# Optimization experiments

Hardware: AMD Instinct MI355X
Metric: run time of the kernel (lower is better)

The kernel has to match this reference:

```python
import jax, jax.numpy as jnp
import numpy as np

N = 4096       # num nodes
E = 131072     # num edges (avg degree 32)
IN = 256
HID = 512
OUT = 64


def _linear_params(k, fan_in, fan_out):
    kw, kb = jax.random.split(k)
    s = 1.0 / np.sqrt(fan_in)
    W = jax.random.uniform(kw, (fan_in, fan_out), jnp.float32, -s, s)
    b = jax.random.uniform(kb, (fan_out,), jnp.float32, -s, s)
    return W, b


def setup_inputs() -> dict:
    key = jax.random.key(0)
    ks = jax.random.split(key, 8)
    x = jax.random.normal(ks[0], (N, IN), jnp.float32)
    edge_index = jax.random.randint(ks[1], (2, E), 0, N, jnp.int32)
    ego_W, ego_b = _linear_params(ks[2], IN, HID)
    cut_W, cut_b = _linear_params(ks[3], IN, HID)
    glob_W, glob_b = _linear_params(ks[4], IN, HID)
    fc_W, fc_b = _linear_params(ks[5], 3 * HID, OUT)
    return dict(x=x, edge_index=edge_index, ego_W=ego_W, ego_b=ego_b,
                cut_W=cut_W, cut_b=cut_b, glob_W=glob_W, glob_b=glob_b,
                fc_W=fc_W, fc_b=fc_b)


def reference(x, edge_index, ego_W, ego_b, cut_W, cut_b, glob_W, glob_b, fc_W, fc_b):
    src, dst = edge_index[0], edge_index[1]
    n = x.shape[0]

    # --- extract_ego_subgraph: mean of x over the unique 2-hop in-neighborhood
    # (k_hop_subgraph flow='source_to_target': walk edges backward), incl. self.
    # B[t, s] = 1 iff edge s -> t exists.
    B = jnp.zeros((n, n), jnp.float32).at[dst, src].set(1.0)
    eye = jnp.eye(n, dtype=jnp.float32)
    reach = ((eye + B + B @ B) > 0).astype(jnp.float32)   # [N, N] bool-as-float
    ego_feat = (reach @ x) / reach.sum(axis=1, keepdims=True)  # counts >= 1 (self)

    # --- extract_cut_subgraph: drop a random half of the edges, then mean of
    # target features over kept out-edges per source node; fallback to x.
    perm = jax.random.permutation(jax.random.key(42), E)
    keep = jnp.ones(E, bool).at[perm[: E // 2]].set(False).astype(x.dtype)  # [E]
    sums = jax.ops.segment_sum(x[dst] * keep[:, None], src, num_segments=n)
    cnt = jax.ops.segment_sum(keep, src, num_segments=n)
    cut_feat = jnp.where((cnt > 0)[:, None], sums / jnp.maximum(cnt, 1.0)[:, None], x)

    # --- MessagePassingLayer: relu(scatter_add(linear(x)[src] -> dst))
    def mp(feat, W, b):
        h = feat @ W + b
        agg = jax.ops.segment_sum(h[src], dst, num_segments=n)
        return jax.nn.relu(agg)

    ego_enc = mp(ego_feat, ego_W, ego_b)
    cut_enc = mp(cut_feat, cut_W, cut_b)
    glob_enc = x @ glob_W + glob_b

    combined = jnp.concatenate([ego_enc, cut_enc, glob_enc], axis=-1)  # [N, 3H]
    out = combined @ fc_W + fc_b
    return jax.nn.log_softmax(out, axis=1)
```

## Files before the change

kernel.cpp:

```cpp
#include <hip/hip_runtime.h>

#define NN 4096
#define NE 131072
#define DIN 256
#define DHID 512
#define DOUT 64
#define DCAT 1536
#define NBINS 65536
#define HALF_E 65536

typedef __attribute__((ext_vector_type(8))) short short8;
typedef __attribute__((ext_vector_type(4))) float f32x4;

__device__ inline unsigned short bf16rne(float f){
  unsigned u = __float_as_uint(f);
  unsigned r = u + 0x7FFFu + ((u>>16)&1u);
  return (unsigned short)(r>>16);
}
__device__ inline float bf2f(unsigned short u){ return __uint_as_float(((unsigned)u)<<16); }

struct K2 { unsigned a, b; };
__host__ __device__ constexpr unsigned rotl32(unsigned x, unsigned d){ return (x<<d)|(x>>(32u-d)); }
__host__ __device__ constexpr K2 tf2x32(unsigned k0, unsigned k1, unsigned x0, unsigned x1){
  unsigned k2 = k0 ^ k1 ^ 0x1BD11BDAu;
  x0 += k0; x1 += k1;
  x0+=x1; x1=rotl32(x1,13); x1^=x0;
  x0+=x1; x1=rotl32(x1,15); x1^=x0;
  x0+=x1; x1=rotl32(x1,26); x1^=x0;
  x0+=x1; x1=rotl32(x1, 6); x1^=x0;
  x0+=k1; x1+=k2+1u;
  x0+=x1; x1=rotl32(x1,17); x1^=x0;
  x0+=x1; x1=rotl32(x1,29); x1^=x0;
  x0+=x1; x1=rotl32(x1,16); x1^=x0;
  x0+=x1; x1=rotl32(x1,24); x1^=x0;
  x0+=k2; x1+=k0+2u;
  x0+=x1; x1=rotl32(x1,13); x1^=x0;
  x0+=x1; x1=rotl32(x1,15); x1^=x0;
  x0+=x1; x1=rotl32(x1,26); x1^=x0;
  x0+=x1; x1=rotl32(x1, 6); x1^=x0;
  x0+=k0; x1+=k1+3u;
  x0+=x1; x1=rotl32(x1,17); x1^=x0;
  x0+=x1; x1=rotl32(x1,29); x1^=x0;
  x0+=x1; x1=rotl32(x1,16); x1^=x0;
  x0+=x1; x1=rotl32(x1,24); x1^=x0;
  x0+=k1; x1+=k2+4u;
  x0+=x1; x1=rotl32(x1,13); x1^=x0;
  x0+=x1; x1=rotl32(x1,15); x1^=x0;
  x0+=x1; x1=rotl32(x1,26); x1^=x0;
  x0+=x1; x1=rotl32(x1, 6); x1^=x0;
  x0+=k2; x1+=k0+5u;
  return K2{x0,x1};
}
static_assert(tf2x32(0u,0u,0u,2u).a==4146024105u, "threefry mismatch o0");
static_assert(tf2x32(0u,0u,0u,2u).b==2718843009u, "threefry mismatch o1");
static_assert(tf2x32(0u,0u,1u,3u).a==967050713u,  "threefry mismatch o0b");
static_assert(tf2x32(0u,0u,1u,3u).b==1272950319u, "threefry mismatch o1b");

constexpr K2 E0 = tf2x32(0u,42u,0u,0u);
constexpr K2 E1 = tf2x32(0u,42u,0u,1u);
constexpr unsigned SK1A = E1.a, SK1B = E1.b;
constexpr K2 F1 = tf2x32(E0.a,E0.b,0u,1u);
constexpr unsigned SK2A = F1.a, SK2B = F1.b;

#define MED_CAP 64

__global__ void genkeysdeg_k(const int* __restrict__ ei,
                             unsigned* __restrict__ keys1, unsigned* __restrict__ keys2,
                             unsigned* __restrict__ hist1, unsigned* __restrict__ hist2,
                             unsigned* __restrict__ indeg, unsigned* __restrict__ outdeg,
                             unsigned* __restrict__ bits){
  unsigned e = blockIdx.x*256u + threadIdx.x;
  K2 r1 = tf2x32(SK1A, SK1B, 0u, e);
  unsigned k1 = r1.a ^ r1.b;
  K2 r2 = tf2x32(SK2A, SK2B, 0u, e);
  unsigned k2 = r2.a ^ r2.b;
  keys1[e] = k1; keys2[e] = k2;
  atomicAdd(&hist1[k1>>16], 1u);
  atomicAdd(&hist2[k2>>16], 1u);
  unsigned s = (unsigned)ei[e], d = (unsigned)ei[NE+e];
  atomicAdd(&outdeg[s], 1u);
  atomicAdd(&indeg[d], 1u);
  atomicOr(&bits[d*128 + (s>>5)], 1u << (s&31));
  if (e < NN) atomicOr(&bits[e*128 + (e>>5)], 1u << (e&31));
}

__global__ void scanA_k(const unsigned* __restrict__ in0, const unsigned* __restrict__ in1,
                        const unsigned* __restrict__ in2, const unsigned* __restrict__ in3,
                        unsigned* __restrict__ o0, unsigned* __restrict__ o1,
                        unsigned* __restrict__ o2, unsigned* __restrict__ o3,
                        unsigned* __restrict__ bsum){
  int y = blockIdx.y;
  int n = (y<2) ? NBINS : NN;
  if ((int)blockIdx.x*256 >= n) return;
  const unsigned* in = y==0?in0 : y==1?in1 : y==2?in2 : in3;
  unsigned* o        = y==0?o0  : y==1?o1  : y==2?o2  : o3;
  __shared__ unsigned s[256];
  int t = threadIdx.x; unsigned i = blockIdx.x*256u + t;
  unsigned v = in[i]; s[t] = v; __syncthreads();
  for (int off=1; off<256; off<<=1){
    unsigned u = (t>=off)?s[t-off]:0u; __syncthreads();
    s[t]+=u; __syncthreads();
  }
  o[i] = s[t]-v;
  if (t==255) bsum[y*256 + blockIdx.x] = s[255];
}
__global__ void scanB_k(unsigned* __restrict__ bsum){
  __shared__ unsigned s[256];
  int y = blockIdx.x, t = threadIdx.x;
  int nb = (y<2) ? 256 : 16;
  unsigned* b = bsum + y*256;
  unsigned v = (t<nb)?b[t]:0u; s[t]=v; __syncthreads();
  for (int off=1; off<256; off<<=1){
    unsigned u=(t>=off)?s[t-off]:0u; __syncthreads();
    s[t]+=u; __syncthreads();
  }
  if (t<nb) b[t]=s[t]-v;
}
__global__ void scanC_k(unsigned* __restrict__ o0, unsigned* __restrict__ o1,
                        unsigned* __restrict__ o2, unsigned* __restrict__ o3,
                        unsigned* __restrict__ c0, unsigned* __restrict__ c1,
                        unsigned* __restrict__ c2, unsigned* __restrict__ c3,
                        const unsigned* __restrict__ bsum){
  int y = blockIdx.y;
  int n = (y<2) ? NBINS : NN;
  if ((int)blockIdx.x*256 >= n) return;
  unsigned* o = y==0?o0 : y==1?o1 : y==2?o2 : o3;
  unsigned* c = y==0?c0 : y==1?c1 : y==2?c2 : c3;
  unsigned i = blockIdx.x*256u + threadIdx.x;
  unsigned v = o[i] + bsum[y*256 + blockIdx.x];
  o[i]=v; c[i]=v;
}

__global__ void med1_k(const unsigned* __restrict__ prefix2, const unsigned* __restrict__ hist2,
                       unsigned* __restrict__ med){
  unsigned h = blockIdx.x*256u + threadIdx.x;
  unsigned p = prefix2[h], n = hist2[h];
  if (p <= HALF_E && HALF_E < p + n){ med[0] = h; med[1] = p; }
}

__global__ void scat1_k(const unsigned* __restrict__ keys1, unsigned* __restrict__ cursor,
                        unsigned* __restrict__ slow, unsigned* __restrict__ stb){
  int e = blockIdx.x*256 + threadIdx.x;
  unsigned k = keys1[e];
  unsigned p = atomicAdd(&cursor[k>>16], 1u);
  slow[p] = k & 0xFFFFu; stb[p] = (unsigned)e;
}
__global__ void rank1_k(const unsigned* __restrict__ keys1, const unsigned* __restrict__ prefix,
                        const unsigned* __restrict__ hist, const unsigned* __restrict__ slow,
                        const unsigned* __restrict__ stb, const unsigned* __restrict__ keys2,
                        unsigned* __restrict__ rank1, unsigned* __restrict__ med){
  int e = blockIdx.x*256 + threadIdx.x;
  unsigned k = keys1[e], h = k>>16, lo = k & 0xFFFFu, tb = (unsigned)e;
  unsigned base = prefix[h], n = hist[h], r = 0;
  for (unsigned j=0;j<n;j++){
    unsigned l2 = slow[base+j], t2 = stb[base+j];
    if (l2 < lo || (l2==lo && t2 < tb)) r++;
  }
  unsigned rk = base + r;
  rank1[e] = rk;
  unsigned k2 = keys2[rk];
  if ((k2>>16) == med[0]){
    unsigned idx = atomicAdd(&med[2], 1u);
    if (idx < MED_CAP){ med[8+idx] = k2 & 0xFFFFu; med[72+idx] = rk; }
  }
}
__global__ void med3_k(unsigned* __restrict__ med){
  int t = threadIdx.x;
  unsigned n = med[2]; if (n > MED_CAP) n = MED_CAP;
  unsigned qcut = HALF_E - med[1];
  if (t < (int)n){
    unsigned lo = med[8+t], rk = med[72+t], pos = 0;
    for (unsigned j=0;j<n;j++){
      unsigned lj = med[8+j], rj = med[72+j];
      if (lj < lo || (lj==lo && rj < rk)) pos++;
    }
    if (pos == qcut){ med[3] = lo; med[4] = rk; }
  }
}

__global__ void scatter_edges_k(const int* __restrict__ ei, const unsigned* __restrict__ rank1,
                                const unsigned* __restrict__ keys2, const unsigned* __restrict__ med,
                                unsigned* __restrict__ curin, unsigned* __restrict__ curout,
                                unsigned* __restrict__ in_list, unsigned* __restrict__ out_list){
  int e = blockIdx.x*256 + threadIdx.x;
  unsigned s = (unsigned)ei[e], d = (unsigned)ei[NE+e];
  unsigned rk = rank1[e], k2 = keys2[rk];
  unsigned h = k2>>16, lo = k2 & 0xFFFFu;
  unsigned hs = med[0], loc = med[3], rkc = med[4];
  unsigned keep = (h > hs) || (h == hs && (lo > loc || (lo == loc && rk >= rkc)));
  unsigned p = atomicAdd(&curin[d], 1u);  in_list[p] = s;
  unsigned q = atomicAdd(&curout[s], 1u); out_list[q] = d | (keep<<31);
}

__global__ void reach_k(const unsigned* __restrict__ bits, const unsigned* __restrict__ in_off,
                        const unsigned* __restrict__ in_list, const unsigned* __restrict__ indeg,
                        unsigned* __restrict__ reach, float* __restrict__ cntinv){
  __shared__ int ws2[2];
  int i = blockIdx.x, t = threadIdx.x;
  unsigned off = in_off[i], deg = indeg[i];
  unsigned acc = bits[i*128 + t];
  for (unsigned j=0;j<deg;j++) acc |= bits[in_list[off+j]*128 + t];
  reach[i*128 + t] = acc;
  int c = __popc(acc);
  for (int o=32;o>0;o>>=1) c += __shfl_xor(c, o, 64);
  if ((t&63)==0) ws2[t>>6] = c;
  __syncthreads();
  if (t==0) cntinv[i] = 1.0f / (float)(ws2[0]+ws2[1]);
}

__device__ inline void tconv(const float* __restrict__ src, unsigned short* __restrict__ dst,
                             int R, int C, int r0, int c0){
  __shared__ unsigned short tile[64][72];
  int t = threadIdx.x;
  int tr = t>>2, tc = (t&3)*16;
  #pragma unroll
  for (int u=0;u<16;u++)
    tile[tr][tc+u] = bf16rne(src[(size_t)(r0+tr)*C + c0 + tc + u]);
  __syncthreads();
  unsigned short v[16];
  #pragma unroll
  for (int u=0;u<16;u++) v[u] = tile[tc+u][tr];
  uint4* vv = (uint4*)v;
  uint4* o = (uint4*)&dst[(size_t)(c0+tr)*R + r0 + tc];
  o[0] = vv[0]; o[1] = vv[1];
}
__global__ void convall_k(const float* __restrict__ x, unsigned short* __restrict__ x_bf,
                          unsigned short* __restrict__ xT_bf,
                          const float* __restrict__ W0, unsigned short* __restrict__ WT0,
                          const float* __restrict__ W1, unsigned short* __restrict__ WT1,
                          const float* __restrict__ W2, unsigned short* __restrict__ WT2,
                          const float* __restrict__ fcW, unsigned short* __restrict__ fcWT){
  int b = blockIdx.x, t = threadIdx.x;
  if (b < 1024){
    int i = b*256 + t;
    float4 f = ((const float4*)x)[i];
    uint2 o;
    o.x = (unsigned)bf16rne(f.x) | ((unsigned)bf16rne(f.y)<<16);
    o.y = (unsigned)bf16rne(f.z) | ((unsigned)bf16rne(f.w)<<16);
    ((uint2*)x_bf)[i] = o;
  } else if (b < 1280){
    int idx = b - 1024;
    tconv(x, xT_bf, NN, DIN, (idx>>2)*64, (idx&3)*64);
  } else if (b < 1376){
    int idx = b - 1280;
    int z = idx >> 5, tl = idx & 31;
    const float* src = z==0?W0 : z==1?W1 : W2;
    unsigned short* dst = z==0?WT0 : z==1?WT1 : WT2;
    tconv(src, dst, DIN, DHID, (tl>>3)*64, (tl&7)*64);
  } else {
    int by = b - 1376;
    tconv(fcW, fcWT, DCAT, DOUT, by*64, 0);
  }
}

__global__ void bitgemm_k(const unsigned* __restrict__ reach, const unsigned short* __restrict__ xT,
                          float* __restrict__ pbuf){
  __shared__ __align__(16) unsigned short bt[4][64*32];
  int t = threadIdx.x, w = t>>6, l = t&63;
  int m0 = blockIdx.x*64, n0 = blockIdx.y*64;
  int kbase = blockIdx.z*(NN/4);
  int srow = t>>2, sg = t&3;
  int arow = m0 + 16*w + (l&15);
  int lg = l>>4;
  f32x4 acc[4];
  #pragma unroll
  for (int c=0;c<4;c++) acc[c] = f32x4{0.f,0.f,0.f,0.f};

  for (int it=0; it<8; ++it){
    int kk = kbase + it*128;
    __syncthreads();
    #pragma unroll
    for (int s=0;s<4;s++){
      uint4 v = *(const uint4*)&xT[(size_t)(n0+srow)*NN + kk + 32*s + sg*8];
      *(uint4*)&bt[s][srow*32 + ((sg ^ (srow&3))*8)] = v;
    }
    __syncthreads();
    unsigned rw[4];
    *(uint4*)rw = *(const uint4*)&reach[(size_t)arow*128 + (kk>>5)];
    #pragma unroll
    for (int s=0;s<4;s++){
      unsigned byte = (rw[s] >> (8*lg)) & 0xFFu;
      union { short8 s8; unsigned u[4]; } af;
      #pragma unroll
      for (int pp=0;pp<4;pp++){
        unsigned b0 = (byte>>(2*pp))&1u, b1 = (byte>>(2*pp+1))&1u;
        af.u[pp] = b0*0x3F80u | b1*0x3F800000u;
      }
      #pragma unroll
      for (int c=0;c<4;c++){
        int brow = 16*c + (l&15);
        short8 bf = *(const short8*)&bt[s][brow*32 + ((lg ^ (brow&3))*8)];
        acc[c] = __builtin_amdgcn_mfma_f32_16x16x32_bf16(af.s8, bf, acc[c], 0,0,0);
      }
    }
  }
  size_t zoff = (size_t)blockIdx.z*NN*DIN;
  #pragma unroll
  for (int c=0;c<4;c++){
    #pragma unroll
    for (int r=0;r<4;r++){
      int row = m0 + 16*w + 4*lg + r;
      int col = n0 + 16*c + (l&15);
      pbuf[zoff + (size_t)row*DIN + col] = acc[c][r];
    }
  }
}

__global__ void redcut_k(const float* __restrict__ pbuf, const float* __restrict__ cntinv,
                         unsigned short* __restrict__ ego_bf,
                         const float* __restrict__ x, const unsigned* __restrict__ out_off,
                         const unsigned* __restrict__ outdeg, const unsigned* __restrict__ out_list,
                         unsigned short* __restrict__ cut_bf){
  int b = blockIdx.x, t = threadIdx.x;
  if (b < 1024){
    int g = b*256 + t;
    const size_t S = (size_t)NN*DIN/4;
    const float4* p4 = (const float4*)pbuf;
    float4 a = p4[g], bb = p4[g+S], c = p4[g+2*S], d = p4[g+3*S];
    int row = (g*4)>>8;
    float ci = cntinv[row];
    float vx = (a.x+bb.x+c.x+d.x)*ci, vy = (a.y+bb.y+c.y+d.y)*ci;
    float vz = (a.z+bb.z+c.z+d.z)*ci, vw = (a.w+bb.w+c.w+d.w)*ci;
    uint2 o;
    o.x = (unsigned)bf16rne(vx) | ((unsigned)bf16rne(vy)<<16);
    o.y = (unsigned)bf16rne(vz) | ((unsigned)bf16rne(vw)<<16);
    ((uint2*)ego_bf)[g] = o;
  } else {
    int s = b - 1024;
    unsigned off = out_off[s], deg = outdeg[s];
    float acc = 0.f; int cnt = 0;
    for (unsigned j=0;j<deg;j++){
      unsigned p = out_list[off+j];
      if (p >> 31){ cnt++; acc += x[(p & 0xFFFFu)*DIN + t]; }
    }
    float v = cnt ? acc / (float)cnt : x[s*DIN + t];
    cut_bf[(size_t)s*DIN + t] = bf16rne(v);
  }
}

__global__ void aggfeat_k(const unsigned short* __restrict__ ego_bf, const unsigned short* __restrict__ cut_bf,
                          const unsigned* __restrict__ in_off, const unsigned* __restrict__ indeg,
                          const unsigned* __restrict__ in_list,
                          unsigned short* __restrict__ aggE, unsigned short* __restrict__ aggC){
  int i = blockIdx.x, t = threadIdx.x;
  unsigned off = in_off[i], deg = indeg[i];
  float ae = 0.f, ac = 0.f;
  for (unsigned j=0;j<deg;j++){
    unsigned s = in_list[off+j];
    ae += bf2f(ego_bf[(size_t)s*DIN + t]);
    ac += bf2f(cut_bf[(size_t)s*DIN + t]);
  }
  aggE[(size_t)i*DIN + t] = bf16rne(ae);
  aggC[(size_t)i*DIN + t] = bf16rne(ac);
}

__global__ void gemm3_k(const unsigned short* __restrict__ aggE, const unsigned short* __restrict__ aggC,
                        const unsigned short* __restrict__ xbf,
                        const unsigned short* __restrict__ WTe, const unsigned short* __restrict__ WTc,
                        const unsigned short* __restrict__ WTg,
                        const float* __restrict__ eb, const float* __restrict__ cb, const float* __restrict__ gb,
                        const unsigned* __restrict__ indeg, unsigned short* __restrict__ hcat){
  __shared__ __align__(16) unsigned short at[4][64*32];
  __shared__ __align__(16) unsigned short bt[4][64*32];
  int z = blockIdx.z;
  const unsigned short* A  = z==0? aggE : z==1? aggC : xbf;
  const unsigned short* BT = z==0? WTe  : z==1? WTc  : WTg;
  const float* bias        = z==0? eb   : z==1? cb   : gb;
  int t = threadIdx.x, w = t>>6, l = t&63;
  int n0 = blockIdx.x*64, m0 = blockIdx.y*64;
  int srow = t>>2, sg = t&3;
  int lg = l>>4;
  f32x4 acc[4];
  #pragma unroll
  for (int c=0;c<4;c++) acc[c] = f32x4{0.f,0.f,0.f,0.f};

  for (int it=0; it<2; ++it){
    int kk = it*128;
    __syncthreads();
    #pragma unroll
    for (int s=0;s<4;s++){
      uint4 va = *(const uint4*)&A [(size_t)(m0+srow)*DIN + kk + 32*s + sg*8];
      uint4 vb = *(const uint4*)&BT[(size_t)(n0+srow)*DIN + kk + 32*s + sg*8];
      *(uint4*)&at[s][srow*32 + ((sg ^ (srow&3))*8)] = va;
      *(uint4*)&bt[s][srow*32 + ((sg ^ (srow&3))*8)] = vb;
    }
    __syncthreads();
    int ar = 16*w + (l&15);
    #pragma unroll
    for (int s=0;s<4;s++){
      short8 af = *(const short8*)&at[s][ar*32 + ((lg ^ (ar&3))*8)];
      #pragma unroll
      for (int c=0;c<4;c++){
        int brow = 16*c + (l&15);
        short8 bf = *(const short8*)&bt[s][brow*32 + ((lg ^ (brow&3))*8)];
        acc[c] = __builtin_amdgcn_mfma_f32_16x16x32_bf16(af, bf, acc[c], 0,0,0);
      }
    }
  }
  #pragma unroll
  for (int c=0;c<4;c++){
    #pragma unroll
    for (int r=0;r<4;r++){
      int row = m0 + 16*w + 4*lg + r;
      int col = n0 + 16*c + (l&15);
      float scale = (z<2) ? (float)indeg[row] : 1.0f;
      float v = acc[c][r] + bias[col]*scale;
      if (z<2) v = fmaxf(v, 0.f);
      hcat[(size_t)row*DCAT + z*DHID + col] = bf16rne(v);
    }
  }
}

__global__ void fcgemm_k(const unsigned short* __restrict__ hcat, const unsigned short* __restrict__ fcWT,
                         float* __restrict__ fcpart){
  __shared__ __align__(16) unsigned short at[4][64*32];
  __shared__ __align__(16) unsigned short bt[4][64*32];
  int t = threadIdx.x, w = t>>6, l = t&63;
  int m0 = blockIdx.x*64;
  int kbase = blockIdx.y*(DCAT/4);
  int srow = t>>2, sg = t&3;
  int lg = l>>4;
  f32x4 acc[4];
  #pragma unroll
  for (int c=0;c<4;c++) acc[c] = f32x4{0.f,0.f,0.f,0.f};

  for (int it=0; it<3; ++it){
    int kk = kbase + it*128;
    __syncthreads();
    #pragma unroll
    for (int s=0;s<4;s++){
      uint4 va = *(const uint4*)&hcat [(size_t)(m0+srow)*DCAT + kk + 32*s + sg*8];
      uint4 vb = *(const uint4*)&fcWT[(size_t)srow*DCAT + kk + 32*s + sg*8];
      *(uint4*)&at[s][srow*32 + ((sg ^ (srow&3))*8)] = va;
      *(uint4*)&bt[s][srow*32 + ((sg ^ (srow&3))*8)] = vb;
    }
    __syncthreads();
    int ar = 16*w + (l&15);
    #pragma unroll
    for (int s=0;s<4;s++){
      short8 af = *(const short8*)&at[s][ar*32 + ((lg ^ (ar&3))*8)];
      #pragma unroll
      for (int c=0;c<4;c++){
        int brow = 16*c + (l&15);
        short8 bf = *(const short8*)&bt[s][brow*32 + ((lg ^ (brow&3))*8)];
        acc[c] = __builtin_amdgcn_mfma_f32_16x16x32_bf16(af, bf, acc[c], 0,0,0);
      }
    }
  }
  size_t zoff = (size_t)blockIdx.y*NN*DOUT;
  #pragma unroll
  for (int c=0;c<4;c++){
    #pragma unroll
    for (int r=0;r<4;r++){
      int row = m0 + 16*w + 4*lg + r;
      int col = 16*c + (l&15);
      fcpart[zoff + (size_t)row*DOUT + col] = acc[c][r];
    }
  }
}

__global__ void fcfin_k(const float* __restrict__ fcpart, const float* __restrict__ fcb,
                        float* __restrict__ out){
  int i = blockIdx.x, l = threadIdx.x;
  const size_t S = (size_t)NN*DOUT;
  size_t idx = (size_t)i*DOUT + l;
  float v = fcpart[idx] + fcpart[idx+S] + fcpart[idx+2*S] + fcpart[idx+3*S] + fcb[l];
  float m = v;
  for (int o=32;o>0;o>>=1) m = fmaxf(m, __shfl_xor(m, o, 64));
  float e = __expf(v - m), s = e;
  for (int o=32;o>0;o>>=1) s += __shfl_xor(s, o, 64);
  out[idx] = (v - m) - logf(s);
}

static inline size_t alignup(size_t x){ return (x + 255) & ~(size_t)255; }

extern "C" void kernel_launch(void* const* d_in, const int* in_sizes, int n_in,
                              void* d_out, int out_size, void* d_ws, size_t ws_size,
                              hipStream_t stream) {
  const float* x      = (const float*)d_in[0];
  const int*   ei     = (const int*)  d_in[1];
  const float* ego_W  = (const float*)d_in[2];
  const float* ego_b  = (const float*)d_in[3];
  const float* cut_W  = (const float*)d_in[4];
  const float* cut_b  = (const float*)d_in[5];
  const float* glob_W = (const float*)d_in[6];
  const float* glob_b = (const float*)d_in[7];
  const float* fc_W   = (const float*)d_in[8];
  const float* fc_b   = (const float*)d_in[9];
  float* out = (float*)d_out;

  char* base = (char*)d_ws;
  char* p = base;
  #define ALLOC(ty, name, cnt) ty* name = (ty*)p; p += alignup(sizeof(ty)*(size_t)(cnt));
  ALLOC(char,           R0,      (size_t)4*NN*DIN*4);
  ALLOC(unsigned,       bits,    NN*128);
  ALLOC(unsigned,       indeg,   NN);
  ALLOC(unsigned,       outdeg,  NN);
  ALLOC(unsigned,       hist1,   NBINS);
  ALLOC(unsigned,       hist2,   NBINS);
  ALLOC(unsigned,       med,     256);
  char* zero_end = p;
  ALLOC(unsigned,       in_off,  NN);
  ALLOC(unsigned,       out_off, NN);
  ALLOC(unsigned,       curin,   NN);
  ALLOC(unsigned,       curout,  NN);
  ALLOC(unsigned,       in_list, NE);
  ALLOC(unsigned,       out_list,NE);
  ALLOC(unsigned,       reach,   NN*128);
  ALLOC(float,          cntinv,  NN);
  ALLOC(unsigned short, x_bf,    (size_t)NN*DIN);
  ALLOC(unsigned short, xT_bf,   (size_t)DIN*NN);
  ALLOC(unsigned short, ego_bf,  (size_t)NN*DIN);
  ALLOC(unsigned short, cut_bf,  (size_t)NN*DIN);
  ALLOC(unsigned short, aggE_bf, (size_t)NN*DIN);
  ALLOC(unsigned short, aggC_bf, (size_t)NN*DIN);
  ALLOC(unsigned short, egoWT,   (size_t)DHID*DIN);
  ALLOC(unsigned short, cutWT,   (size_t)DHID*DIN);
  ALLOC(unsigned short, globWT,  (size_t)DHID*DIN);
  ALLOC(unsigned short, fcWT,    (size_t)DOUT*DCAT);
  ALLOC(unsigned,       prefix1, NBINS);
  ALLOC(unsigned,       cursor1, NBINS);
  ALLOC(unsigned,       prefix2, NBINS);
  ALLOC(unsigned,       cursor2, NBINS);
  ALLOC(unsigned,       bsum,    1024);
  ALLOC(float,          fcpart,  (size_t)4*NN*DOUT);
  #undef ALLOC
  size_t need = (size_t)(p - base);
  if (ws_size < need){
    hipMemsetAsync(d_out, 0x7F, (size_t)out_size*sizeof(float), stream);
    return;
  }
  float*          pbuf = (float*)R0;
  unsigned short* hcat = (unsigned short*)R0;
  char* q = R0;
  #define OALLOC(ty, name, cnt) ty* name = (ty*)q; q += alignup(sizeof(ty)*(size_t)(cnt));
  OALLOC(unsigned, keys1,  NE);
  OALLOC(unsigned, keys2,  NE);
  OALLOC(unsigned, rank1,  NE);
  OALLOC(unsigned, slow,   NE);
  OALLOC(unsigned, stb,    NE);
  #undef OALLOC

  const int EB = NE/256;

  hipMemsetAsync(bits, 0, (size_t)(zero_end - (char*)bits), stream);
  hipLaunchKernelGGL(genkeysdeg_k, dim3(EB), dim3(256), 0, stream,
                     ei, keys1, keys2, hist1, hist2, indeg, outdeg, bits);
  hipLaunchKernelGGL(scanA_k, dim3(NBINS/256, 4), dim3(256), 0, stream,
                     hist1, hist2, indeg, outdeg, prefix1, prefix2, in_off, out_off, bsum);
  hipLaunchKernelGGL(scanB_k, dim3(4), dim3(256), 0, stream, bsum);
  hipLaunchKernelGGL(scanC_k, dim3(NBINS/256, 4), dim3(256), 0, stream,
                     prefix1, prefix2, in_off, out_off, cursor1, cursor2, curin, curout, bsum);
  hipLaunchKernelGGL(med1_k, dim3(NBINS/256), dim3(256), 0, stream, prefix2, hist2, med);
  hipLaunchKernelGGL(scat1_k, dim3(EB), dim3(256), 0, stream, keys1, cursor1, slow, stb);
  hipLaunchKernelGGL(rank1_k, dim3(EB), dim3(256), 0, stream,
                     keys1, prefix1, hist1, slow, stb, keys2, rank1, med);
  hipLaunchKernelGGL(med3_k, dim3(1), dim3(64), 0, stream, med);
  hipLaunchKernelGGL(scatter_edges_k, dim3(EB), dim3(256), 0, stream,
                     ei, rank1, keys2, med, curin, curout, in_list, out_list);
  hipLaunchKernelGGL(reach_k, dim3(NN), dim3(128), 0, stream,
                     bits, in_off, in_list, indeg, reach, cntinv);
  hipLaunchKernelGGL(convall_k, dim3(1400), dim3(256), 0, stream,
                     x, x_bf, xT_bf, ego_W, egoWT, cut_W, cutWT, glob_W, globWT, fc_W, fcWT);
  hipLaunchKernelGGL(bitgemm_k, dim3(NN/64, DIN/64, 4), dim3(256), 0, stream, reach, xT_bf, pbuf);
  hipLaunchKernelGGL(redcut_k, dim3(5120), dim3(256), 0, stream,
                     pbuf, cntinv, ego_bf, x, out_off, outdeg, out_list, cut_bf);
  hipLaunchKernelGGL(aggfeat_k, dim3(NN), dim3(256), 0, stream,
                     ego_bf, cut_bf, in_off, indeg, in_list, aggE_bf, aggC_bf);
  hipLaunchKernelGGL(gemm3_k, dim3(DHID/64, NN/64, 3), dim3(256), 0, stream,
                     aggE_bf, aggC_bf, x_bf, egoWT, cutWT, globWT,
                     ego_b, cut_b, glob_b, indeg, hcat);
  hipLaunchKernelGGL(fcgemm_k, dim3(NN/64, 4), dim3(256), 0, stream, hcat, fcWT, fcpart);
  hipLaunchKernelGGL(fcfin_k, dim3(NN), dim3(64), 0, stream, fcpart, fc_b, out);
}
```

Measured before the change: 193.0 us.

## Fuse front-end kernels and replace three-pass scan with single-pass lookback

Folds the random-key and degree kernel together with the bf16 conversion and transpose kernel into one launch. The three-kernel scan plus the separate median search becomes one decoupled-lookback scan. Median-candidate collection moves into the scatter kernel, and the median select runs as an extra block of the rank kernel. The cut-feature mean is fused with the reachability kernel, leaving a separate scale kernel for the ego features. The aim is to cut launch count and serialization, at the cost of relying on lookback spin-waits making forward progress and on tie-break semantics that now use the edge index.

```diff
diff --git a/kernel.cpp b/kernel.cpp
--- a/kernel.cpp
+++ b/kernel.cpp
@@ -64,118 +64,162 @@
 
 #define MED_CAP 64
 
-__global__ void genkeysdeg_k(const int* __restrict__ ei,
-                             unsigned* __restrict__ keys1, unsigned* __restrict__ keys2,
-                             unsigned* __restrict__ hist1, unsigned* __restrict__ hist2,
-                             unsigned* __restrict__ indeg, unsigned* __restrict__ outdeg,
-                             unsigned* __restrict__ bits){
-  unsigned e = blockIdx.x*256u + threadIdx.x;
-  K2 r1 = tf2x32(SK1A, SK1B, 0u, e);
-  unsigned k1 = r1.a ^ r1.b;
-  K2 r2 = tf2x32(SK2A, SK2B, 0u, e);
-  unsigned k2 = r2.a ^ r2.b;
-  keys1[e] = k1; keys2[e] = k2;
-  atomicAdd(&hist1[k1>>16], 1u);
-  atomicAdd(&hist2[k2>>16], 1u);
-  unsigned s = (unsigned)ei[e], d = (unsigned)ei[NE+e];
-  atomicAdd(&outdeg[s], 1u);
-  atomicAdd(&indeg[d], 1u);
-  atomicOr(&bits[d*128 + (s>>5)], 1u << (s&31));
-  if (e < NN) atomicOr(&bits[e*128 + (e>>5)], 1u << (e&31));
-}
-
-__global__ void scanA_k(const unsigned* __restrict__ in0, const unsigned* __restrict__ in1,
-                        const unsigned* __restrict__ in2, const unsigned* __restrict__ in3,
-                        unsigned* __restrict__ o0, unsigned* __restrict__ o1,
-                        unsigned* __restrict__ o2, unsigned* __restrict__ o3,
-                        unsigned* __restrict__ bsum){
+__device__ inline void tconv(const float* __restrict__ src, unsigned short* __restrict__ dst,
+                             int R, int C, int r0, int c0){
+  __shared__ unsigned short tile[64][72];
+  int t = threadIdx.x;
+  int tr = t>>2, tc = (t&3)*16;
+  #pragma unroll
+  for (int u=0;u<16;u++)
+    tile[tr][tc+u] = bf16rne(src[(size_t)(r0+tr)*C + c0 + tc + u]);
+  __syncthreads();
+  unsigned short v[16];
+  #pragma unroll
+  for (int u=0;u<16;u++) v[u] = tile[tc+u][tr];
+  uint4* vv = (uint4*)v;
+  uint4* o = (uint4*)&dst[(size_t)(c0+tr)*R + r0 + tc];
+  o[0] = vv[0]; o[1] = vv[1];
+}
+
+__global__ void front_k(const int* __restrict__ ei,
+                        unsigned* __restrict__ keys1, unsigned* __restrict__ keys2,
+                        unsigned* __restrict__ hist1, unsigned* __restrict__ hist2,
+                        unsigned* __restrict__ indeg, unsigned* __restrict__ outdeg,
+                        unsigned* __restrict__ bits,
+                        const float* __restrict__ x, unsigned short* __restrict__ x_bf,
+                        unsigned short* __restrict__ xT_bf,
+                        const float* __restrict__ W0, unsigned short* __restrict__ WT0,
+                        const float* __restrict__ W1, unsigned short* __restrict__ WT1,
+                        const float* __restrict__ W2, unsigned short* __restrict__ WT2,
+                        const float* __restrict__ fcW, unsigned short* __restrict__ fcWT){
+  int b = blockIdx.x, t = threadIdx.x;
+  if (b < 512){
+    unsigned e = b*256u + t;
+    K2 r1 = tf2x32(SK1A, SK1B, 0u, e);
+    unsigned k1 = r1.a ^ r1.b;
+    K2 r2 = tf2x32(SK2A, SK2B, 0u, e);
+    unsigned k2 = r2.a ^ r2.b;
+    keys1[e] = k1; keys2[e] = k2;
+    atomicAdd(&hist1[k1>>16], 1u);
+    atomicAdd(&hist2[k2>>16], 1u);
+    unsigned s = (unsigned)ei[e], d = (unsigned)ei[NE+e];
+    atomicAdd(&outdeg[s], 1u);
+    atomicAdd(&indeg[d], 1u);
+    atomicOr(&bits[d*128 + (s>>5)], 1u << (s&31));
+    if (e < NN) atomicOr(&bits[e*128 + (e>>5)], 1u << (e&31));
+    return;
+  }
+  int b2 = b - 512;
+  if (b2 < 1024){
+    int i = b2*256 + t;
+    float4 f = ((const float4*)x)[i];
+    uint2 o;
+    o.x = (unsigned)bf16rne(f.x) | ((unsigned)bf16rne(f.y)<<16);
+    o.y = (unsigned)bf16rne(f.z) | ((unsigned)bf16rne(f.w)<<16);
+    ((uint2*)x_bf)[i] = o;
+  } else if (b2 < 1280){
+    int idx = b2 - 1024;
+    tconv(x, xT_bf, NN, DIN, (idx>>2)*64, (idx&3)*64);
+  } else if (b2 < 1376){
+    int idx = b2 - 1280;
+    int z = idx >> 5, tl = idx & 31;
+    const float* src = z==0?W0 : z==1?W1 : W2;
+    unsigned short* dst = z==0?WT0 : z==1?WT1 : WT2;
+    tconv(src, dst, DIN, DHID, (tl>>3)*64, (tl&7)*64);
+  } else {
+    int by = b2 - 1376;
+    tconv(fcW, fcWT, DCAT, DOUT, by*64, 0);
+  }
+}
+
+__global__ void scanAll_k(const unsigned* __restrict__ in0, const unsigned* __restrict__ in1,
+                          const unsigned* __restrict__ in2, const unsigned* __restrict__ in3,
+                          unsigned* __restrict__ o0, unsigned* __restrict__ o1,
+                          unsigned* __restrict__ o2, unsigned* __restrict__ o3,
+                          unsigned* __restrict__ c0, unsigned* __restrict__ c1,
+                          unsigned* __restrict__ c2, unsigned* __restrict__ c3,
+                          unsigned* __restrict__ flags, unsigned* __restrict__ med){
   int y = blockIdx.y;
-  int n = (y<2) ? NBINS : NN;
-  if ((int)blockIdx.x*256 >= n) return;
+  int nblk = (y<2) ? (NBINS/256) : (NN/256);
+  int xb = blockIdx.x;
+  if (xb >= nblk) return;
   const unsigned* in = y==0?in0 : y==1?in1 : y==2?in2 : in3;
   unsigned* o        = y==0?o0  : y==1?o1  : y==2?o2  : o3;
+  unsigned* c        = y==0?c0  : y==1?c1  : y==2?c2  : c3;
   __shared__ unsigned s[256];
-  int t = threadIdx.x; unsigned i = blockIdx.x*256u + t;
+  __shared__ unsigned base_s;
+  int t = threadIdx.x; unsigned i = xb*256u + t;
   unsigned v = in[i]; s[t] = v; __syncthreads();
   for (int off=1; off<256; off<<=1){
     unsigned u = (t>=off)?s[t-off]:0u; __syncthreads();
     s[t]+=u; __syncthreads();
   }
-  o[i] = s[t]-v;
-  if (t==255) bsum[y*256 + blockIdx.x] = s[255];
-}
-__global__ void scanB_k(unsigned* __restrict__ bsum){
-  __shared__ unsigned s[256];
-  int y = blockIdx.x, t = threadIdx.x;
-  int nb = (y<2) ? 256 : 16;
-  unsigned* b = bsum + y*256;
-  unsigned v = (t<nb)?b[t]:0u; s[t]=v; __syncthreads();
-  for (int off=1; off<256; off<<=1){
-    unsigned u=(t>=off)?s[t-off]:0u; __syncthreads();
-    s[t]+=u; __syncthreads();
-  }
-  if (t<nb) b[t]=s[t]-v;
-}
-__global__ void scanC_k(unsigned* __restrict__ o0, unsigned* __restrict__ o1,
-                        unsigned* __restrict__ o2, unsigned* __restrict__ o3,
-                        unsigned* __restrict__ c0, unsigned* __restrict__ c1,
-                        unsigned* __restrict__ c2, unsigned* __restrict__ c3,
-                        const unsigned* __restrict__ bsum){
-  int y = blockIdx.y;
-  int n = (y<2) ? NBINS : NN;
-  if ((int)blockIdx.x*256 >= n) return;
-  unsigned* o = y==0?o0 : y==1?o1 : y==2?o2 : o3;
-  unsigned* c = y==0?c0 : y==1?c1 : y==2?c2 : c3;
-  unsigned i = blockIdx.x*256u + threadIdx.x;
-  unsigned v = o[i] + bsum[y*256 + blockIdx.x];
-  o[i]=v; c[i]=v;
-}
-
-__global__ void med1_k(const unsigned* __restrict__ prefix2, const unsigned* __restrict__ hist2,
-                       unsigned* __restrict__ med){
-  unsigned h = blockIdx.x*256u + threadIdx.x;
-  unsigned p = prefix2[h], n = hist2[h];
-  if (p <= HALF_E && HALF_E < p + n){ med[0] = h; med[1] = p; }
-}
-
-__global__ void scat1_k(const unsigned* __restrict__ keys1, unsigned* __restrict__ cursor,
-                        unsigned* __restrict__ slow, unsigned* __restrict__ stb){
+  unsigned excl = s[t]-v;
+  unsigned total = s[255];
+  if (t==0){
+    unsigned* f = flags + y*256;
+    if (xb==0){
+      atomicExch(&f[0], 0x80000000u | total);
+      base_s = 0u;
+    } else {
+      atomicExch(&f[xb], 0x40000000u | total);
+      unsigned base = 0u; int pr = xb-1;
+      while (true){
+        unsigned fv = atomicAdd(&f[pr], 0u);
+        if (fv & 0x80000000u){ base += fv & 0x3FFFFFFFu; break; }
+        if (fv & 0x40000000u){ base += fv & 0x3FFFFFFFu; pr--; continue; }
+        __builtin_amdgcn_s_sleep(1);
+      }
+      atomicExch(&f[xb], 0x80000000u | (base + total));
+      base_s = base;
+    }
+  }
+  __syncthreads();
+  unsigned res = excl + base_s;
+  o[i] = res; c[i] = res;
+  if (y==1 && res <= HALF_E && HALF_E < res + v){ med[0] = i; med[1] = res; }
+}
+
+__global__ void scat1med_k(const unsigned* __restrict__ keys1, const unsigned* __restrict__ keys2,
+                           unsigned* __restrict__ cursor, unsigned* __restrict__ slow,
+                           unsigned* __restrict__ stb, unsigned* __restrict__ med){
   int e = blockIdx.x*256 + threadIdx.x;
   unsigned k = keys1[e];
   unsigned p = atomicAdd(&cursor[k>>16], 1u);
   slow[p] = k & 0xFFFFu; stb[p] = (unsigned)e;
-}
-__global__ void rank1_k(const unsigned* __restrict__ keys1, const unsigned* __restrict__ prefix,
-                        const unsigned* __restrict__ hist, const unsigned* __restrict__ slow,
-                        const unsigned* __restrict__ stb, const unsigned* __restrict__ keys2,
-                        unsigned* __restrict__ rank1, unsigned* __restrict__ med){
-  int e = blockIdx.x*256 + threadIdx.x;
+  unsigned k2 = keys2[e];
+  if ((k2>>16) == med[0]){
+    unsigned idx = atomicAdd(&med[2], 1u);
+    if (idx < MED_CAP){ med[8+idx] = k2 & 0xFFFFu; med[72+idx] = (unsigned)e; }
+  }
+}
+
+__global__ void rank1med_k(const unsigned* __restrict__ keys1, const unsigned* __restrict__ prefix,
+                           const unsigned* __restrict__ hist, const unsigned* __restrict__ slow,
+                           const unsigned* __restrict__ stb, unsigned* __restrict__ rank1,
+                           unsigned* __restrict__ med){
+  int b = blockIdx.x, t = threadIdx.x;
+  if (b == NE/256){
+    unsigned n = med[2]; if (n > MED_CAP) n = MED_CAP;
+    unsigned qcut = HALF_E - med[1];
+    if (t < (int)n){
+      unsigned lo = med[8+t], rk = med[72+t], pos = 0;
+      for (unsigned j=0;j<n;j++){
+        unsigned lj = med[8+j], rj = med[72+j];
+        if (lj < lo || (lj==lo && rj < rk)) pos++;
+      }
+      if (pos == qcut){ med[3] = lo; med[4] = rk; }
+    }
+    return;
+  }
+  int e = b*256 + t;
   unsigned k = keys1[e], h = k>>16, lo = k & 0xFFFFu, tb = (unsigned)e;
   unsigned base = prefix[h], n = hist[h], r = 0;
   for (unsigned j=0;j<n;j++){
     unsigned l2 = slow[base+j], t2 = stb[base+j];
     if (l2 < lo || (l2==lo && t2 < tb)) r++;
   }
-  unsigned rk = base + r;
-  rank1[e] = rk;
-  unsigned k2 = keys2[rk];
-  if ((k2>>16) == med[0]){
-    unsigned idx = atomicAdd(&med[2], 1u);
-    if (idx < MED_CAP){ med[8+idx] = k2 & 0xFFFFu; med[72+idx] = rk; }
-  }
-}
-__global__ void med3_k(unsigned* __restrict__ med){
-  int t = threadIdx.x;
-  unsigned n = med[2]; if (n > MED_CAP) n = MED_CAP;
-  unsigned qcut = HALF_E - med[1];
-  if (t < (int)n){
-    unsigned lo = med[8+t], rk = med[72+t], pos = 0;
-    for (unsigned j=0;j<n;j++){
-      unsigned lj = med[8+j], rj = med[72+j];
-      if (lj < lo || (lj==lo && rj < rk)) pos++;
-    }
-    if (pos == qcut){ med[3] = lo; med[4] = rk; }
-  }
+  rank1[e] = base + r;
 }
 
 __global__ void scatter_edges_k(const int* __restrict__ ei, const unsigned* __restrict__ rank1,
@@ -192,64 +236,38 @@
   unsigned q = atomicAdd(&curout[s], 1u); out_list[q] = d | (keep<<31);
 }
 
-__global__ void reach_k(const unsigned* __restrict__ bits, const unsigned* __restrict__ in_off,
-                        const unsigned* __restrict__ in_list, const unsigned* __restrict__ indeg,
-                        unsigned* __restrict__ reach, float* __restrict__ cntinv){
-  __shared__ int ws2[2];
-  int i = blockIdx.x, t = threadIdx.x;
-  unsigned off = in_off[i], deg = indeg[i];
-  unsigned acc = bits[i*128 + t];
-  for (unsigned j=0;j<deg;j++) acc |= bits[in_list[off+j]*128 + t];
-  reach[i*128 + t] = acc;
-  int c = __popc(acc);
-  for (int o=32;o>0;o>>=1) c += __shfl_xor(c, o, 64);
-  if ((t&63)==0) ws2[t>>6] = c;
-  __syncthreads();
-  if (t==0) cntinv[i] = 1.0f / (float)(ws2[0]+ws2[1]);
-}
-
-__device__ inline void tconv(const float* __restrict__ src, unsigned short* __restrict__ dst,
-                             int R, int C, int r0, int c0){
-  __shared__ unsigned short tile[64][72];
-  int t = threadIdx.x;
-  int tr = t>>2, tc = (t&3)*16;
-  #pragma unroll
-  for (int u=0;u<16;u++)
-    tile[tr][tc+u] = bf16rne(src[(size_t)(r0+tr)*C + c0 + tc + u]);
-  __syncthreads();
-  unsigned short v[16];
-  #pragma unroll
-  for (int u=0;u<16;u++) v[u] = tile[tc+u][tr];
-  uint4* vv = (uint4*)v;
-  uint4* o = (uint4*)&dst[(size_t)(c0+tr)*R + r0 + tc];
-  o[0] = vv[0]; o[1] = vv[1];
-}
-__global__ void convall_k(const float* __restrict__ x, unsigned short* __restrict__ x_bf,
-                          unsigned short* __restrict__ xT_bf,
-                          const float* __restrict__ W0, unsigned short* __restrict__ WT0,
-                          const float* __restrict__ W1, unsigned short* __restrict__ WT1,
-                          const float* __restrict__ W2, unsigned short* __restrict__ WT2,
-                          const float* __restrict__ fcW, unsigned short* __restrict__ fcWT){
+__global__ void reachcut_k(const unsigned* __restrict__ bits, const unsigned* __restrict__ in_off,
+                           const unsigned* __restrict__ in_list, const unsigned* __restrict__ indeg,
+                           unsigned* __restrict__ reach, float* __restrict__ cntinv,
+                           const float* __restrict__ x, const unsigned* __restrict__ out_off,
+                           const unsigned* __restrict__ outdeg, const unsigned* __restrict__ out_list,
+                           unsigned short* __restrict__ cut_bf){
   int b = blockIdx.x, t = threadIdx.x;
-  if (b < 1024){
-    int i = b*256 + t;
-    float4 f = ((const float4*)x)[i];
-    uint2 o;
-    o.x = (unsigned)bf16rne(f.x) | ((unsigned)bf16rne(f.y)<<16);
-    o.y = (unsigned)bf16rne(f.z) | ((unsigned)bf16rne(f.w)<<16);
-    ((uint2*)x_bf)[i] = o;
-  } else if (b < 1280){
-    int idx = b - 1024;
-    tconv(x, xT_bf, NN, DIN, (idx>>2)*64, (idx&3)*64);
-  } else if (b < 1376){
-    int idx = b - 1280;
-    int z = idx >> 5, tl = idx & 31;
-    const float* src = z==0?W0 : z==1?W1 : W2;
-    unsigned short* dst = z==0?WT0 : z==1?WT1 : WT2;
-    tconv(src, dst, DIN, DHID, (tl>>3)*64, (tl&7)*64);
+  if (b < NN){
+    __shared__ int ws4[4];
+    int i = b;
+    int c = 0;
+    if (t < 128){
+      unsigned off = in_off[i], deg = indeg[i];
+      unsigned acc = bits[i*128 + t];
+      for (unsigned j=0;j<deg;j++) acc |= bits[in_list[off+j]*128 + t];
+      reach[i*128 + t] = acc;
+      c = __popc(acc);
+    }
+    for (int o=32;o>0;o>>=1) c += __shfl_xor(c, o, 64);
+    if ((t&63)==0) ws4[t>>6] = c;
+    __syncthreads();
+    if (t==0) cntinv[i] = 1.0f / (float)(ws4[0]+ws4[1]+ws4[2]+ws4[3]);
   } else {
-    int by = b - 1376;
-    tconv(fcW, fcWT, DCAT, DOUT, by*64, 0);
+    int s = b - NN;
+    unsigned off = out_off[s], deg = outdeg[s];
+    float acc = 0.f; int cnt = 0;
+    for (unsigned j=0;j<deg;j++){
+      unsigned p = out_list[off+j];
+      if (p >> 31){ cnt++; acc += x[(p & 0xFFFFu)*DIN + t]; }
+    }
+    float v = cnt ? acc / (float)cnt : x[s*DIN + t];
+    cut_bf[(size_t)s*DIN + t] = bf16rne(v);
   }
 }
 
@@ -306,36 +324,20 @@
   }
 }
 
-__global__ void redcut_k(const float* __restrict__ pbuf, const float* __restrict__ cntinv,
-                         unsigned short* __restrict__ ego_bf,
-                         const float* __restrict__ x, const unsigned* __restrict__ out_off,
-                         const unsigned* __restrict__ outdeg, const unsigned* __restrict__ out_list,
-                         unsigned short* __restrict__ cut_bf){
-  int b = blockIdx.x, t = threadIdx.x;
-  if (b < 1024){
-    int g = b*256 + t;
-    const size_t S = (size_t)NN*DIN/4;
-    const float4* p4 = (const float4*)pbuf;
-    float4 a = p4[g], bb = p4[g+S], c = p4[g+2*S], d = p4[g+3*S];
-    int row = (g*4)>>8;
-    float ci = cntinv[row];
-    float vx = (a.x+bb.x+c.x+d.x)*ci, vy = (a.y+bb.y+c.y+d.y)*ci;
-    float vz = (a.z+bb.z+c.z+d.z)*ci, vw = (a.w+bb.w+c.w+d.w)*ci;
-    uint2 o;
-    o.x = (unsigned)bf16rne(vx) | ((unsigned)bf16rne(vy)<<16);
-    o.y = (unsigned)bf16rne(vz) | ((unsigned)bf16rne(vw)<<16);
-    ((uint2*)ego_bf)[g] = o;
-  } else {
-    int s = b - 1024;
-    unsigned off = out_off[s], deg = outdeg[s];
-    float acc = 0.f; int cnt = 0;
-    for (unsigned j=0;j<deg;j++){
-      unsigned p = out_list[off+j];
-      if (p >> 31){ cnt++; acc += x[(p & 0xFFFFu)*DIN + t]; }
-    }
-    float v = cnt ? acc / (float)cnt : x[s*DIN + t];
-    cut_bf[(size_t)s*DIN + t] = bf16rne(v);
-  }
+__global__ void redscale_k(const float* __restrict__ pbuf, const float* __restrict__ cntinv,
+                           unsigned short* __restrict__ ego_bf){
+  int g = blockIdx.x*256 + threadIdx.x;
+  const size_t S = (size_t)NN*DIN/4;
+  const float4* p4 = (const float4*)pbuf;
+  float4 a = p4[g], b = p4[g+S], c = p4[g+2*S], d = p4[g+3*S];
+  int row = (g*4)>>8;
+  float ci = cntinv[row];
+  float vx = (a.x+b.x+c.x+d.x)*ci, vy = (a.y+b.y+c.y+d.y)*ci;
+  float vz = (a.z+b.z+c.z+d.z)*ci, vw = (a.w+b.w+c.w+d.w)*ci;
+  uint2 o;
+  o.x = (unsigned)bf16rne(vx) | ((unsigned)bf16rne(vy)<<16);
+  o.y = (unsigned)bf16rne(vz) | ((unsigned)bf16rne(vw)<<16);
+  ((uint2*)ego_bf)[g] = o;
 }
 
 __global__ void aggfeat_k(const unsigned short* __restrict__ ego_bf, const unsigned short* __restrict__ cut_bf,
@@ -499,6 +501,7 @@
   ALLOC(unsigned,       hist1,   NBINS);
   ALLOC(unsigned,       hist2,   NBINS);
   ALLOC(unsigned,       med,     256);
+  ALLOC(unsigned,       flags,   1024);
   char* zero_end = p;
   ALLOC(unsigned,       in_off,  NN);
   ALLOC(unsigned,       out_off, NN);
@@ -522,7 +525,6 @@
   ALLOC(unsigned,       cursor1, NBINS);
   ALLOC(unsigned,       prefix2, NBINS);
   ALLOC(unsigned,       cursor2, NBINS);
-  ALLOC(unsigned,       bsum,    1024);
   ALLOC(float,          fcpart,  (size_t)4*NN*DOUT);
   #undef ALLOC
   size_t need = (size_t)(p - base);
@@ -544,27 +546,24 @@
   const int EB = NE/256;
 
   hipMemsetAsync(bits, 0, (size_t)(zero_end - (char*)bits), stream);
-  hipLaunchKernelGGL(genkeysdeg_k, dim3(EB), dim3(256), 0, stream,
-                     ei, keys1, keys2, hist1, hist2, indeg, outdeg, bits);
-  hipLaunchKernelGGL(scanA_k, dim3(NBINS/256, 4), dim3(256), 0, stream,
-                     hist1, hist2, indeg, outdeg, prefix1, prefix2, in_off, out_off, bsum);
-  hipLaunchKernelGGL(scanB_k, dim3(4), dim3(256), 0, stream, bsum);
-  hipLaunchKernelGGL(scanC_k, dim3(NBINS/256, 4), dim3(256), 0, stream,
-                     prefix1, prefix2, in_off, out_off, cursor1, cursor2, curin, curout, bsum);
-  hipLaunchKernelGGL(med1_k, dim3(NBINS/256), dim3(256), 0, stream, prefix2, hist2, med);
-  hipLaunchKernelGGL(scat1_k, dim3(EB), dim3(256), 0, stream, keys1, cursor1, slow, stb);
-  hipLaunchKernelGGL(rank1_k, dim3(EB), dim3(256), 0, stream,
-                     keys1, prefix1, hist1, slow, stb, keys2, rank1, med);
-  hipLaunchKernelGGL(med3_k, dim3(1), dim3(64), 0, stream, med);
+  hipLaunchKernelGGL(front_k, dim3(1912), dim3(256), 0, stream,
+                     ei, keys1, keys2, hist1, hist2, indeg, outdeg, bits,
+                     x, x_bf, xT_bf, ego_W, egoWT, cut_W, cutWT, glob_W, globWT, fc_W, fcWT);
+  hipLaunchKernelGGL(scanAll_k, dim3(NBINS/256, 4), dim3(256), 0, stream,
+                     hist1, hist2, indeg, outdeg,
+                     prefix1, prefix2, in_off, out_off,
+                     cursor1, cursor2, curin, curout, flags, med);
+  hipLaunchKernelGGL(scat1med_k, dim3(EB), dim3(256), 0, stream,
+                     keys1, keys2, cursor1, slow, stb, med);
+  hipLaunchKernelGGL(rank1med_k, dim3(EB+1), dim3(256), 0, stream,
+                     keys1, prefix1, hist1, slow, stb, rank1, med);
   hipLaunchKernelGGL(scatter_edges_k, dim3(EB), dim3(256), 0, stream,
                      ei, rank1, keys2, med, curin, curout, in_list, out_list);
-  hipLaunchKernelGGL(reach_k, dim3(NN), dim3(128), 0, stream,
-                     bits, in_off, in_list, indeg, reach, cntinv);
-  hipLaunchKernelGGL(convall_k, dim3(1400), dim3(256), 0, stream,
-                     x, x_bf, xT_bf, ego_W, egoWT, cut_W, cutWT, glob_W, globWT, fc_W, fcWT);
+  hipLaunchKernelGGL(reachcut_k, dim3(2*NN), dim3(256), 0, stream,
+                     bits, in_off, in_list, indeg, reach, cntinv,
+                     x, out_off, outdeg, out_list, cut_bf);
   hipLaunchKernelGGL(bitgemm_k, dim3(NN/64, DIN/64, 4), dim3(256), 0, stream, reach, xT_bf, pbuf);
-  hipLaunchKernelGGL(redcut_k, dim3(5120), dim3(256), 0, stream,
-                     pbuf, cntinv, ego_bf, x, out_off, outdeg, out_list, cut_bf);
+  hipLaunchKernelGGL(redscale_k, dim3((NN*DIN/4)/256), dim3(256), 0, stream, pbuf, cntinv, ego_bf);
   hipLaunchKernelGGL(aggfeat_k, dim3(NN), dim3(256), 0, stream,
                      ego_bf, cut_bf, in_off, indeg, in_list, aggE_bf, aggC_bf);
   hipLaunchKernelGGL(gemm3_k, dim3(DHID/64, NN/64, 3), dim3(256), 0, stream,
```

New measurement: 203.4 us. 1.05x slower.
